# Performance work log

Hardware: AMD Instinct MI355X
Metric: run time of the kernel (lower is better)

The kernel has to match this reference:

```python
import jax, jax.numpy as jnp
import numpy as np

QP = 127.0          # signed symmetric 8-bit: Qp = 2**(8-1)-1
MIN_RANGE = 1e-6


def _ste_round(q):
    # round_pass: straight-through estimator round
    return q + jax.lax.stop_gradient(jnp.round(q) - q)


def _quant_per_token(x):
    # symmetric per-token: amax over last dim, keepdim
    s = jnp.clip(jnp.max(jnp.abs(x), axis=-1, keepdims=True), MIN_RANGE, None) / QP
    return _ste_round(x / s), s


def _quant_per_tensor(w):
    s = jnp.clip(jnp.max(jnp.abs(w)), MIN_RANGE, None) / QP
    return _ste_round(w / s), s


def _qlinear(x2d, w, b):
    # fake-quant linear: quantize act per-token, weight per-tensor,
    # int-domain matmul, bias added before dequant rescale (faithful to source)
    qx, sx = _quant_per_token(x2d)      # [N,K], [N,1]
    qw, sw = _quant_per_tensor(w)       # [M,K], scalar
    out = jnp.matmul(qx, qw.T) + b[None, :]
    return out * (sx * sw)              # [N,M]


def setup_inputs() -> dict:
    key = jax.random.key(0)
    k1, k2, k3, k4, k5 = jax.random.split(key, 5)
    B, S, D, H = 64, 197, 768, 3072
    return {
        "x": jax.random.normal(k1, (B, S, D), dtype=jnp.float32),
        "w1": jax.random.normal(k2, (H, D), dtype=jnp.float32) * 0.02,
        "b1": jax.random.normal(k3, (H,), dtype=jnp.float32) * 0.02,
        "w2": jax.random.normal(k4, (D, H), dtype=jnp.float32) * 0.02,
        "b2": jax.random.normal(k5, (D,), dtype=jnp.float32) * 0.02,
    }


def reference(x, w1, b1, w2, b2):
    B, S, D = x.shape
    x2d = x.reshape(-1, D)                         # view(-1, x.size(-1))
    h = _qlinear(x2d, w1, b1)                      # fc1
    h = jax.nn.gelu(h, approximate=False)          # ViT Mlp activation (exact GELU)
    o = _qlinear(h, w2, b2)                        # fc2
    return o.reshape(B, S, -1)
```

## Files before the change

### kernel.cpp

```cpp
#include <hip/hip_runtime.h>
#include <stdint.h>

#define QPF  127.0f
#define MINR 1e-6f

typedef int v4i __attribute__((ext_vector_type(4)));
typedef float f4v __attribute__((ext_vector_type(4)));
typedef _Float16 h4v __attribute__((ext_vector_type(4)));
typedef _Float16 h8 __attribute__((ext_vector_type(8)));
typedef signed char c8 __attribute__((ext_vector_type(8)));

__device__ __forceinline__ float wave_max64(float v) {
  v = fmaxf(v, __shfl_xor(v, 32, 64));
  v = fmaxf(v, __shfl_xor(v, 16, 64));
  v = fmaxf(v, __shfl_xor(v, 8, 64));
  v = fmaxf(v, __shfl_xor(v, 4, 64));
  v = fmaxf(v, __shfl_xor(v, 2, 64));
  v = fmaxf(v, __shfl_xor(v, 1, 64));
  return v;
}

__device__ __forceinline__ float gelu_exact(float x) {
  float z = fabsf(x) * 0.70710678118654752440f;
  float t = __builtin_amdgcn_rcpf(fmaf(0.3275911f, z, 1.0f));
  float p = fmaf(fmaf(fmaf(fmaf(1.061405429f, t, -1.453152027f), t,
                           1.421413741f), t, -0.284496736f), t, 0.254829592f) * t;
  float e = __expf(-z * z);
  float erfz = fmaf(-p, e, 1.0f);
  float cdf = fmaf(0.5f, copysignf(erfz, x), 0.5f);
  return x * cdf;
}

__device__ __forceinline__ void gl2lds16(const void* g, void* l) {
  __builtin_amdgcn_global_load_lds(
      (const __attribute__((address_space(1))) int*)g,
      (__attribute__((address_space(3))) int*)l,
      16, 0, 0);
}

__device__ __forceinline__ int xcd_swizzle(int flat, int nwg) {
  const int xcd = flat & 7;
  const int idx = flat >> 3;
  const int q = nwg >> 3, r = nwg & 7;
  const int base = (xcd < r) ? xcd * (q + 1) : r * (q + 1) + (xcd - r) * q;
  return base + idx;
}

__global__ __launch_bounds__(256) void pre_kernel(
    const float* __restrict__ w1, const float* __restrict__ w2, int n4,
    const float* __restrict__ x, signed char* __restrict__ qx,
    float* __restrict__ sx, unsigned* __restrict__ amaxh,
    float* __restrict__ partial, int K, int nTok) {
  __shared__ float red[4];
  const int b = blockIdx.x;
  const int tid = threadIdx.x;
  const int lane = tid & 63, wvi = tid >> 6;

  if (b < 1024) {
    const float4* w4 = (const float4*)(b < 512 ? w1 : w2);
    const int bb = b & 511;
    float m = 0.f;
    for (int i = bb * 256 + tid; i < n4; i += 512 * 256) {
      float4 v = w4[i];
      m = fmaxf(m, fmaxf(fmaxf(fabsf(v.x), fabsf(v.y)),
                         fmaxf(fabsf(v.z), fabsf(v.w))));
    }
    m = wave_max64(m);
    if (lane == 0) red[wvi] = m;
    __syncthreads();
    if (tid == 0)
      partial[b] = fmaxf(fmaxf(red[0], red[1]), fmaxf(red[2], red[3]));
  } else {
    const int token = (b - 1024) * 4 + wvi;
    if (token < nTok) {
      const int k4 = K >> 2;
      const float4* xr = (const float4*)(x + (size_t)token * K);
      float m = 0.f;
      for (int i = lane; i < k4; i += 64) {
        float4 v = xr[i];
        m = fmaxf(m, fmaxf(fmaxf(fabsf(v.x), fabsf(v.y)),
                           fmaxf(fabsf(v.z), fabsf(v.w))));
      }
      m = wave_max64(m);
      const float s = fmaxf(m, MINR) / QPF;
      const float rs = 1.0f / s;
      if (lane == 0) { sx[token] = s; amaxh[token] = 0u; }
      char4* q4 = (char4*)(qx + (size_t)token * K);
      for (int i = lane; i < k4; i += 64) {
        float4 v = xr[i];
        char4 c;
        c.x = (signed char)(int)rintf(v.x * rs);
        c.y = (signed char)(int)rintf(v.y * rs);
        c.z = (signed char)(int)rintf(v.z * rs);
        c.w = (signed char)(int)rintf(v.w * rs);
        q4[i] = c;
      }
    }
  }
}

__global__ __launch_bounds__(256) void wquant2_kernel(
    const float* __restrict__ w1, const float* __restrict__ w2, int n4,
    const float* __restrict__ partial, unsigned* __restrict__ wamax,
    signed char* __restrict__ q1, signed char* __restrict__ q2) {
  __shared__ float red[4];
  const int tid = threadIdx.x;
  const int lane = tid & 63, wvi = tid >> 6;
  const int y = blockIdx.y;
  float m = fmaxf(partial[y * 512 + tid], partial[y * 512 + 256 + tid]);
  m = wave_max64(m);
  if (lane == 0) red[wvi] = m;
  __syncthreads();
  const float M = fmaxf(fmaxf(red[0], red[1]), fmaxf(red[2], red[3]));
  if (blockIdx.x == 0 && tid == 0) wamax[y] = __float_as_uint(M);
  const float s = fmaxf(M, MINR) / QPF;
  const float rs = 1.0f / s;
  const float4* w4 = (const float4*)(y ? w2 : w1);
  char4* q4 = (char4*)(y ? q2 : q1);
  for (int i = blockIdx.x * 256 + tid; i < n4; i += gridDim.x * 256) {
    float4 v = w4[i];
    char4 c;
    c.x = (signed char)(int)rintf(v.x * rs);
    c.y = (signed char)(int)rintf(v.y * rs);
    c.z = (signed char)(int)rintf(v.z * rs);
    c.w = (signed char)(int)rintf(v.w * rs);
    q4[i] = c;
  }
}

__global__ __launch_bounds__(256) void hquant4_kernel(
    const _Float16* __restrict__ h, const unsigned* __restrict__ amaxbits,
    signed char* __restrict__ qh, float* __restrict__ sh, int K) {
  const int token = blockIdx.x * 4 + (threadIdx.x >> 6);
  const int lane = threadIdx.x & 63;
  const float s = fmaxf(__uint_as_float(amaxbits[token]), MINR) / QPF;
  const float rs = 1.0f / s;
  if (lane == 0) sh[token] = s;
  const h8* hr = (const h8*)(h + (size_t)token * K);
  c8* qr = (c8*)(qh + (size_t)token * K);
  for (int i = lane; i < (K >> 3); i += 64) {
    h8 v = hr[i];
    c8 c;
#pragma unroll
    for (int j = 0; j < 8; j++)
      c[j] = (signed char)(int)rintf((float)v[j] * rs);
    qr[i] = c;
  }
}

__global__ __launch_bounds__(256, 2) void gemm1_i8(
    const signed char* __restrict__ A, const signed char* __restrict__ B,
    const float* __restrict__ bias, const float* __restrict__ sA,
    const unsigned* __restrict__ sBbits, _Float16* __restrict__ out,
    unsigned* __restrict__ amax_out, int N, int K, int Mout) {
  __shared__ __align__(16) signed char lds[3 * 16384];

  const int t = threadIdx.x;
  const int lane = t & 63;
  const int wv = t >> 6;
  const int wm = wv >> 1;
  const int wn = wv & 1;

  const int nwg = gridDim.x * gridDim.y;
  const int wg = xcd_swizzle(blockIdx.x + gridDim.x * blockIdx.y, nwg);
  const int colBlk = (wg % gridDim.x) * 128;
  const int rowBlk = (wg / gridDim.x) * 128;

  int ar0 = rowBlk + wv * 16 + (lane >> 2);
  int ar1 = ar0 + 64;
  if (ar0 > N - 1) ar0 = N - 1;
  if (ar1 > N - 1) ar1 = N - 1;
  const int br0 = colBlk + wv * 16 + (lane >> 2);
  const int br1 = br0 + 64;
  const int kb = (((lane & 3) ^ ((lane >> 3) & 3)) * 16);

  const signed char* gA0 = A + (size_t)ar0 * K + kb;
  const signed char* gA1 = A + (size_t)ar1 * K + kb;
  const signed char* gB0 = B + (size_t)br0 * K + kb;
  const signed char* gB1 = B + (size_t)br1 * K + kb;

  const v4i vzero = {0, 0, 0, 0};
  v4i acc[4][4];
#pragma unroll
  for (int i = 0; i < 4; i++)
#pragma unroll
    for (int j = 0; j < 4; j++) acc[i][j] = vzero;

  const int swz = ((lane >> 4) ^ ((lane >> 1) & 3)) * 16;
  const int aoff = (wm * 64 + (lane & 15)) * 64 + swz;
  const int boff = (wn * 64 + (lane & 15)) * 64 + swz + 8192;

  const int T = K >> 6;

  auto issue = [&](int bufo) {
    signed char* a = lds + bufo + wv * 1024;
    gl2lds16(gA0, a);
    gl2lds16(gA1, a + 4096);
    gl2lds16(gB0, a + 8192);
    gl2lds16(gB1, a + 12288);
    gA0 += 64; gA1 += 64; gB0 += 64; gB1 += 64;
  };

  issue(0);
  issue(16384);

  int cur = 0;
  for (int kt = 0; kt < T; ++kt) {
    asm volatile("" ::: "memory");
    if (kt < T - 1)
      __builtin_amdgcn_s_waitcnt(0x0074);
    else
      __builtin_amdgcn_s_waitcnt(0x0070);
    __builtin_amdgcn_s_barrier();
    asm volatile("" ::: "memory");

    if (kt + 2 < T) {
      int pf = cur + 32768;
      if (pf >= 49152) pf -= 49152;
      issue(pf);
    }

    v4i a[4], b[4];
#pragma unroll
    for (int mi = 0; mi < 4; mi++)
      a[mi] = *(const v4i*)(lds + cur + aoff + mi * 1024);
#pragma unroll
    for (int ni = 0; ni < 4; ni++)
      b[ni] = *(const v4i*)(lds + cur + boff + ni * 1024);
#pragma unroll
    for (int mi = 0; mi < 4; mi++)
#pragma unroll
      for (int ni = 0; ni < 4; ni++)
        acc[mi][ni] = __builtin_amdgcn_mfma_i32_16x16x64_i8(b[ni], a[mi],
                                                            acc[mi][ni], 0, 0, 0);
    cur += 16384;
    if (cur >= 49152) cur = 0;
  }

  const float sB = fmaxf(__uint_as_float(*sBbits), MINR) / QPF;
  const int col0 = colBlk + wn * 64 + (lane >> 4) * 4;

  f4v bv[4];
#pragma unroll
  for (int ni = 0; ni < 4; ni++) bv[ni] = *(const f4v*)(bias + col0 + ni * 16);

#pragma unroll
  for (int mi = 0; mi < 4; mi++) {
    const int grow = rowBlk + wm * 64 + mi * 16 + (lane & 15);
    const float ss = ((grow < N) ? sA[grow] : 0.f) * sB;
    float rmax = 0.f;
#pragma unroll
    for (int ni = 0; ni < 4; ni++) {
      h4v hv;
#pragma unroll
      for (int r = 0; r < 4; r++) {
        float v = ((float)acc[mi][ni][r] + bv[ni][r]) * ss;
        v = gelu_exact(v);
        rmax = fmaxf(rmax, fabsf(v));
        hv[r] = (_Float16)v;
      }
      if (grow < N)
        *(h4v*)(out + (size_t)grow * Mout + col0 + ni * 16) = hv;
    }
    rmax = fmaxf(rmax, __shfl_xor(rmax, 16, 64));
    rmax = fmaxf(rmax, __shfl_xor(rmax, 32, 64));
    if (lane < 16 && grow < N)
      atomicMax(amax_out + grow, __float_as_uint(rmax));
  }
}

__global__ __launch_bounds__(256, 2) void gemm2_i8(
    const signed char* __restrict__ A, const signed char* __restrict__ B,
    const float* __restrict__ bias, const float* __restrict__ sA,
    const unsigned* __restrict__ sBbits, float* __restrict__ out,
    int N, int K, int Mout) {
  __shared__ __align__(16) signed char lds[3 * 16384];

  const int t = threadIdx.x;
  const int lane = t & 63;
  const int wv = t >> 6;
  const int wm = wv >> 1;
  const int wn = wv & 1;

  const int nwg = gridDim.x * gridDim.y;
  const int wg = xcd_swizzle(blockIdx.x + gridDim.x * blockIdx.y, nwg);
  const int colBlk = (wg % gridDim.x) * 128;
  const int rowBlk = (wg / gridDim.x) * 128;

  int ar0 = rowBlk + wv * 16 + (lane >> 2);
  int ar1 = ar0 + 64;
  if (ar0 > N - 1) ar0 = N - 1;
  if (ar1 > N - 1) ar1 = N - 1;
  const int br0 = colBlk + wv * 16 + (lane >> 2);
  const int br1 = br0 + 64;
  const int kb = (((lane & 3) ^ ((lane >> 3) & 3)) * 16);

  const signed char* gA0 = A + (size_t)ar0 * K + kb;
  const signed char* gA1 = A + (size_t)ar1 * K + kb;
  const signed char* gB0 = B + (size_t)br0 * K + kb;
  const signed char* gB1 = B + (size_t)br1 * K + kb;

  const v4i vzero = {0, 0, 0, 0};
  v4i acc[4][4];
#pragma unroll
  for (int i = 0; i < 4; i++)
#pragma unroll
    for (int j = 0; j < 4; j++) acc[i][j] = vzero;

  const int swz = ((lane >> 4) ^ ((lane >> 1) & 3)) * 16;
  const int aoff = (wm * 64 + (lane & 15)) * 64 + swz;
  const int boff = (wn * 64 + (lane & 15)) * 64 + swz + 8192;

  const int T = K >> 6;

  auto issue = [&](int bufo) {
    signed char* a = lds + bufo + wv * 1024;
    gl2lds16(gA0, a);
    gl2lds16(gA1, a + 4096);
    gl2lds16(gB0, a + 8192);
    gl2lds16(gB1, a + 12288);
    gA0 += 64; gA1 += 64; gB0 += 64; gB1 += 64;
  };

  issue(0);
  issue(16384);

  int cur = 0;
  for (int kt = 0; kt < T; ++kt) {
    asm volatile("" ::: "memory");
    if (kt < T - 1)
      __builtin_amdgcn_s_waitcnt(0x0074);
    else
      __builtin_amdgcn_s_waitcnt(0x0070);
    __builtin_amdgcn_s_barrier();
    asm volatile("" ::: "memory");

    if (kt + 2 < T) {
      int pf = cur + 32768;
      if (pf >= 49152) pf -= 49152;
      issue(pf);
    }

    v4i a[4], b[4];
#pragma unroll
    for (int mi = 0; mi < 4; mi++)
      a[mi] = *(const v4i*)(lds + cur + aoff + mi * 1024);
#pragma unroll
    for (int ni = 0; ni < 4; ni++)
      b[ni] = *(const v4i*)(lds + cur + boff + ni * 1024);
#pragma unroll
    for (int mi = 0; mi < 4; mi++)
#pragma unroll
      for (int ni = 0; ni < 4; ni++)
        acc[mi][ni] = __builtin_amdgcn_mfma_i32_16x16x64_i8(b[ni], a[mi],
                                                            acc[mi][ni], 0, 0, 0);
    cur += 16384;
    if (cur >= 49152) cur = 0;
  }

  const float sB = fmaxf(__uint_as_float(*sBbits), MINR) / QPF;
  const int col0 = colBlk + wn * 64 + (lane >> 4) * 4;

  f4v bv[4];
#pragma unroll
  for (int ni = 0; ni < 4; ni++) bv[ni] = *(const f4v*)(bias + col0 + ni * 16);

#pragma unroll
  for (int mi = 0; mi < 4; mi++) {
    const int grow = rowBlk + wm * 64 + mi * 16 + (lane & 15);
    const float ss = ((grow < N) ? sA[grow] : 0.f) * sB;
#pragma unroll
    for (int ni = 0; ni < 4; ni++) {
      f4v o;
#pragma unroll
      for (int r = 0; r < 4; r++)
        o[r] = ((float)acc[mi][ni][r] + bv[ni][r]) * ss;
      if (grow < N)
        *(f4v*)(out + (size_t)grow * Mout + col0 + ni * 16) = o;
    }
  }
}

extern "C" void kernel_launch(void* const* d_in, const int* in_sizes, int n_in,
                              void* d_out, int out_size, void* d_ws, size_t ws_size,
                              hipStream_t stream) {
  const float* x  = (const float*)d_in[0];
  const float* w1 = (const float*)d_in[1];
  const float* b1 = (const float*)d_in[2];
  const float* w2 = (const float*)d_in[3];
  const float* b2 = (const float*)d_in[4];

  const int H = in_sizes[2];
  const int D = in_sizes[4];
  const int N = in_sizes[0] / D;
  float* out = (float*)d_out;

  char* ws = (char*)d_ws;
  auto alloc = [&](size_t bytes) {
    char* p = ws;
    ws += (bytes + 255) & ~(size_t)255;
    return p;
  };
  signed char* qx  = (signed char*)alloc((size_t)N * D);
  signed char* qw1 = (signed char*)alloc((size_t)H * D);
  signed char* qw2 = (signed char*)alloc((size_t)H * D);
  signed char* qh  = (signed char*)alloc((size_t)N * H);
  float*    sx     = (float*)alloc((size_t)N * 4);
  float*    sh     = (float*)alloc((size_t)N * 4);
  unsigned* amaxh  = (unsigned*)alloc((size_t)N * 4);
  unsigned* wamax  = (unsigned*)alloc(256);
  float*    partial= (float*)alloc(1024 * 4);
  _Float16* h      = (_Float16*)alloc((size_t)N * H * 2);
  (void)ws_size;

  const int n4w = (H * D) >> 2;

  pre_kernel<<<1024 + (N + 3) / 4, 256, 0, stream>>>(w1, w2, n4w, x, qx, sx,
                                                     amaxh, partial, D, N);
  wquant2_kernel<<<dim3(512, 2), 256, 0, stream>>>(w1, w2, n4w, partial, wamax,
                                                   qw1, qw2);

  dim3 g1(H / 128, (N + 127) / 128);
  gemm1_i8<<<g1, 256, 0, stream>>>(qx, qw1, b1, sx, wamax + 0, h, amaxh,
                                   N, D, H);
  hquant4_kernel<<<N / 4, 256, 0, stream>>>(h, amaxh, qh, sh, H);

  dim3 g2(D / 128, (N + 127) / 128);
  gemm2_i8<<<g2, 256, 0, stream>>>(qh, qw2, b2, sh, wamax + 1, out, N, H, D);
}
```

Before: 234.3 us.

## Enlarge int8 GEMM tiles to 128x256 and 256x128 with six-load staging

```diff
diff --git a/kernel.cpp b/kernel.cpp
--- a/kernel.cpp
+++ b/kernel.cpp
@@ -153,7 +153,7 @@
     const float* __restrict__ bias, const float* __restrict__ sA,
     const unsigned* __restrict__ sBbits, _Float16* __restrict__ out,
     unsigned* __restrict__ amax_out, int N, int K, int Mout) {
-  __shared__ __align__(16) signed char lds[3 * 16384];
+  __shared__ __align__(16) signed char lds[3 * 24576];
 
   const int t = threadIdx.x;
   const int lane = t & 63;
@@ -163,86 +163,92 @@
 
   const int nwg = gridDim.x * gridDim.y;
   const int wg = xcd_swizzle(blockIdx.x + gridDim.x * blockIdx.y, nwg);
-  const int colBlk = (wg % gridDim.x) * 128;
+  const int colBlk = (wg % gridDim.x) * 256;
   const int rowBlk = (wg / gridDim.x) * 128;
 
-  int ar0 = rowBlk + wv * 16 + (lane >> 2);
-  int ar1 = ar0 + 64;
-  if (ar0 > N - 1) ar0 = N - 1;
-  if (ar1 > N - 1) ar1 = N - 1;
-  const int br0 = colBlk + wv * 16 + (lane >> 2);
-  const int br1 = br0 + 64;
   const int kb = (((lane & 3) ^ ((lane >> 3) & 3)) * 16);
-
-  const signed char* gA0 = A + (size_t)ar0 * K + kb;
-  const signed char* gA1 = A + (size_t)ar1 * K + kb;
-  const signed char* gB0 = B + (size_t)br0 * K + kb;
-  const signed char* gB1 = B + (size_t)br1 * K + kb;
+  const int rr = lane >> 2;
+
+  const signed char* gp[6];
+  int ldo[6];
+#pragma unroll
+  for (int j = 0; j < 6; j++) {
+    const int c = wv + 4 * j;
+    if (c < 8) {
+      int r = rowBlk + c * 16 + rr;
+      if (r > N - 1) r = N - 1;
+      gp[j] = A + (size_t)r * K + kb;
+      ldo[j] = c * 1024;
+    } else {
+      const int r = colBlk + (c - 8) * 16 + rr;
+      gp[j] = B + (size_t)r * K + kb;
+      ldo[j] = 8192 + (c - 8) * 1024;
+    }
+  }
 
   const v4i vzero = {0, 0, 0, 0};
-  v4i acc[4][4];
+  v4i acc[4][8];
 #pragma unroll
   for (int i = 0; i < 4; i++)
 #pragma unroll
-    for (int j = 0; j < 4; j++) acc[i][j] = vzero;
+    for (int j = 0; j < 8; j++) acc[i][j] = vzero;
 
   const int swz = ((lane >> 4) ^ ((lane >> 1) & 3)) * 16;
   const int aoff = (wm * 64 + (lane & 15)) * 64 + swz;
-  const int boff = (wn * 64 + (lane & 15)) * 64 + swz + 8192;
+  const int boff = 8192 + (wn * 128 + (lane & 15)) * 64 + swz;
 
   const int T = K >> 6;
 
   auto issue = [&](int bufo) {
-    signed char* a = lds + bufo + wv * 1024;
-    gl2lds16(gA0, a);
-    gl2lds16(gA1, a + 4096);
-    gl2lds16(gB0, a + 8192);
-    gl2lds16(gB1, a + 12288);
-    gA0 += 64; gA1 += 64; gB0 += 64; gB1 += 64;
+#pragma unroll
+    for (int j = 0; j < 6; j++) {
+      gl2lds16(gp[j], lds + bufo + ldo[j]);
+      gp[j] += 64;
+    }
   };
 
   issue(0);
-  issue(16384);
+  issue(24576);
 
   int cur = 0;
   for (int kt = 0; kt < T; ++kt) {
     asm volatile("" ::: "memory");
     if (kt < T - 1)
-      __builtin_amdgcn_s_waitcnt(0x0074);
+      __builtin_amdgcn_s_waitcnt(0x0076);
     else
       __builtin_amdgcn_s_waitcnt(0x0070);
     __builtin_amdgcn_s_barrier();
     asm volatile("" ::: "memory");
 
     if (kt + 2 < T) {
-      int pf = cur + 32768;
-      if (pf >= 49152) pf -= 49152;
+      int pf = cur + 49152;
+      if (pf >= 73728) pf -= 73728;
       issue(pf);
     }
 
-    v4i a[4], b[4];
+    v4i a[4], b[8];
 #pragma unroll
     for (int mi = 0; mi < 4; mi++)
       a[mi] = *(const v4i*)(lds + cur + aoff + mi * 1024);
 #pragma unroll
-    for (int ni = 0; ni < 4; ni++)
+    for (int ni = 0; ni < 8; ni++)
       b[ni] = *(const v4i*)(lds + cur + boff + ni * 1024);
 #pragma unroll
     for (int mi = 0; mi < 4; mi++)
 #pragma unroll
-      for (int ni = 0; ni < 4; ni++)
+      for (int ni = 0; ni < 8; ni++)
         acc[mi][ni] = __builtin_amdgcn_mfma_i32_16x16x64_i8(b[ni], a[mi],
                                                             acc[mi][ni], 0, 0, 0);
-    cur += 16384;
-    if (cur >= 49152) cur = 0;
+    cur += 24576;
+    if (cur >= 73728) cur = 0;
   }
 
   const float sB = fmaxf(__uint_as_float(*sBbits), MINR) / QPF;
-  const int col0 = colBlk + wn * 64 + (lane >> 4) * 4;
-
-  f4v bv[4];
-#pragma unroll
-  for (int ni = 0; ni < 4; ni++) bv[ni] = *(const f4v*)(bias + col0 + ni * 16);
+  const int col0 = colBlk + wn * 128 + (lane >> 4) * 4;
+
+  f4v bv[8];
+#pragma unroll
+  for (int ni = 0; ni < 8; ni++) bv[ni] = *(const f4v*)(bias + col0 + ni * 16);
 
 #pragma unroll
   for (int mi = 0; mi < 4; mi++) {
@@ -250,7 +256,7 @@
     const float ss = ((grow < N) ? sA[grow] : 0.f) * sB;
     float rmax = 0.f;
 #pragma unroll
-    for (int ni = 0; ni < 4; ni++) {
+    for (int ni = 0; ni < 8; ni++) {
       h4v hv;
 #pragma unroll
       for (int r = 0; r < 4; r++) {
@@ -274,7 +280,7 @@
     const float* __restrict__ bias, const float* __restrict__ sA,
     const unsigned* __restrict__ sBbits, float* __restrict__ out,
     int N, int K, int Mout) {
-  __shared__ __align__(16) signed char lds[3 * 16384];
+  __shared__ __align__(16) signed char lds[3 * 24576];
 
   const int t = threadIdx.x;
   const int lane = t & 63;
@@ -285,77 +291,83 @@
   const int nwg = gridDim.x * gridDim.y;
   const int wg = xcd_swizzle(blockIdx.x + gridDim.x * blockIdx.y, nwg);
   const int colBlk = (wg % gridDim.x) * 128;
-  const int rowBlk = (wg / gridDim.x) * 128;
-
-  int ar0 = rowBlk + wv * 16 + (lane >> 2);
-  int ar1 = ar0 + 64;
-  if (ar0 > N - 1) ar0 = N - 1;
-  if (ar1 > N - 1) ar1 = N - 1;
-  const int br0 = colBlk + wv * 16 + (lane >> 2);
-  const int br1 = br0 + 64;
+  const int rowBlk = (wg / gridDim.x) * 256;
+
   const int kb = (((lane & 3) ^ ((lane >> 3) & 3)) * 16);
-
-  const signed char* gA0 = A + (size_t)ar0 * K + kb;
-  const signed char* gA1 = A + (size_t)ar1 * K + kb;
-  const signed char* gB0 = B + (size_t)br0 * K + kb;
-  const signed char* gB1 = B + (size_t)br1 * K + kb;
+  const int rr = lane >> 2;
+
+  const signed char* gp[6];
+  int ldo[6];
+#pragma unroll
+  for (int j = 0; j < 6; j++) {
+    const int c = wv + 4 * j;
+    if (c < 16) {
+      int r = rowBlk + c * 16 + rr;
+      if (r > N - 1) r = N - 1;
+      gp[j] = A + (size_t)r * K + kb;
+      ldo[j] = c * 1024;
+    } else {
+      const int r = colBlk + (c - 16) * 16 + rr;
+      gp[j] = B + (size_t)r * K + kb;
+      ldo[j] = 16384 + (c - 16) * 1024;
+    }
+  }
 
   const v4i vzero = {0, 0, 0, 0};
-  v4i acc[4][4];
-#pragma unroll
-  for (int i = 0; i < 4; i++)
+  v4i acc[8][4];
+#pragma unroll
+  for (int i = 0; i < 8; i++)
 #pragma unroll
     for (int j = 0; j < 4; j++) acc[i][j] = vzero;
 
   const int swz = ((lane >> 4) ^ ((lane >> 1) & 3)) * 16;
-  const int aoff = (wm * 64 + (lane & 15)) * 64 + swz;
-  const int boff = (wn * 64 + (lane & 15)) * 64 + swz + 8192;
+  const int aoff = (wm * 128 + (lane & 15)) * 64 + swz;
+  const int boff = 16384 + (wn * 64 + (lane & 15)) * 64 + swz;
 
   const int T = K >> 6;
 
   auto issue = [&](int bufo) {
-    signed char* a = lds + bufo + wv * 1024;
-    gl2lds16(gA0, a);
-    gl2lds16(gA1, a + 4096);
-    gl2lds16(gB0, a + 8192);
-    gl2lds16(gB1, a + 12288);
-    gA0 += 64; gA1 += 64; gB0 += 64; gB1 += 64;
+#pragma unroll
+    for (int j = 0; j < 6; j++) {
+      gl2lds16(gp[j], lds + bufo + ldo[j]);
+      gp[j] += 64;
+    }
   };
 
   issue(0);
-  issue(16384);
+  issue(24576);
 
   int cur = 0;
   for (int kt = 0; kt < T; ++kt) {
     asm volatile("" ::: "memory");
     if (kt < T - 1)
-      __builtin_amdgcn_s_waitcnt(0x0074);
+      __builtin_amdgcn_s_waitcnt(0x0076);
     else
       __builtin_amdgcn_s_waitcnt(0x0070);
     __builtin_amdgcn_s_barrier();
     asm volatile("" ::: "memory");
 
     if (kt + 2 < T) {
-      int pf = cur + 32768;
-      if (pf >= 49152) pf -= 49152;
+      int pf = cur + 49152;
+      if (pf >= 73728) pf -= 73728;
       issue(pf);
     }
 
-    v4i a[4], b[4];
-#pragma unroll
-    for (int mi = 0; mi < 4; mi++)
+    v4i a[8], b[4];
+#pragma unroll
+    for (int mi = 0; mi < 8; mi++)
       a[mi] = *(const v4i*)(lds + cur + aoff + mi * 1024);
 #pragma unroll
     for (int ni = 0; ni < 4; ni++)
       b[ni] = *(const v4i*)(lds + cur + boff + ni * 1024);
 #pragma unroll
-    for (int mi = 0; mi < 4; mi++)
+    for (int mi = 0; mi < 8; mi++)
 #pragma unroll
       for (int ni = 0; ni < 4; ni++)
         acc[mi][ni] = __builtin_amdgcn_mfma_i32_16x16x64_i8(b[ni], a[mi],
                                                             acc[mi][ni], 0, 0, 0);
-    cur += 16384;
-    if (cur >= 49152) cur = 0;
+    cur += 24576;
+    if (cur >= 73728) cur = 0;
   }
 
   const float sB = fmaxf(__uint_as_float(*sBbits), MINR) / QPF;
@@ -366,8 +378,8 @@
   for (int ni = 0; ni < 4; ni++) bv[ni] = *(const f4v*)(bias + col0 + ni * 16);
 
 #pragma unroll
-  for (int mi = 0; mi < 4; mi++) {
-    const int grow = rowBlk + wm * 64 + mi * 16 + (lane & 15);
+  for (int mi = 0; mi < 8; mi++) {
+    const int grow = rowBlk + wm * 128 + mi * 16 + (lane & 15);
     const float ss = ((grow < N) ? sA[grow] : 0.f) * sB;
 #pragma unroll
     for (int ni = 0; ni < 4; ni++) {
@@ -420,11 +432,11 @@
   wquant2_kernel<<<dim3(512, 2), 256, 0, stream>>>(w1, w2, n4w, partial, wamax,
                                                    qw1, qw2);
 
-  dim3 g1(H / 128, (N + 127) / 128);
+  dim3 g1(H / 256, (N + 127) / 128);
   gemm1_i8<<<g1, 256, 0, stream>>>(qx, qw1, b1, sx, wamax + 0, h, amaxh,
                                    N, D, H);
   hquant4_kernel<<<N / 4, 256, 0, stream>>>(h, amaxh, qh, sh, H);
 
-  dim3 g2(D / 128, (N + 127) / 128);
+  dim3 g2(D / 128, (N + 255) / 256);
   gemm2_i8<<<g2, 256, 0, stream>>>(qh, qw2, b2, sh, wamax + 1, out, N, H, D);
 }
```

New measurement: 238.6 us. About the same (+1.8%).

## Replace LDS-staged triple buffering with direct global-to-register double-buffered loads

Applied to the files above, without the earlier changes.

```diff
diff --git a/kernel.cpp b/kernel.cpp
--- a/kernel.cpp
+++ b/kernel.cpp
@@ -29,13 +29,6 @@
   float erfz = fmaf(-p, e, 1.0f);
   float cdf = fmaf(0.5f, copysignf(erfz, x), 0.5f);
   return x * cdf;
-}
-
-__device__ __forceinline__ void gl2lds16(const void* g, void* l) {
-  __builtin_amdgcn_global_load_lds(
-      (const __attribute__((address_space(1))) int*)g,
-      (__attribute__((address_space(3))) int*)l,
-      16, 0, 0);
 }
 
 __device__ __forceinline__ int xcd_swizzle(int flat, int nwg) {
@@ -148,13 +141,23 @@
   }
 }
 
+#define GLOADF(XA, WB, KB)                                        \
+  _Pragma("unroll") for (int i_ = 0; i_ < 4; i_++)                \
+      XA[i_] = *(const v4i*)(A + aofs[i_] + (KB));                \
+  _Pragma("unroll") for (int i_ = 0; i_ < 4; i_++)                \
+      WB[i_] = *(const v4i*)(B + bofs[i_] + (KB));
+
+#define GMMA(XA, WB)                                              \
+  _Pragma("unroll") for (int mi_ = 0; mi_ < 4; mi_++)             \
+  _Pragma("unroll") for (int ni_ = 0; ni_ < 4; ni_++)             \
+      acc[mi_][ni_] = __builtin_amdgcn_mfma_i32_16x16x64_i8(      \
+          WB[ni_], XA[mi_], acc[mi_][ni_], 0, 0, 0);
+
 __global__ __launch_bounds__(256, 2) void gemm1_i8(
     const signed char* __restrict__ A, const signed char* __restrict__ B,
     const float* __restrict__ bias, const float* __restrict__ sA,
     const unsigned* __restrict__ sBbits, _Float16* __restrict__ out,
     unsigned* __restrict__ amax_out, int N, int K, int Mout) {
-  __shared__ __align__(16) signed char lds[3 * 16384];
-
   const int t = threadIdx.x;
   const int lane = t & 63;
   const int wv = t >> 6;
@@ -166,18 +169,20 @@
   const int colBlk = (wg % gridDim.x) * 128;
   const int rowBlk = (wg / gridDim.x) * 128;
 
-  int ar0 = rowBlk + wv * 16 + (lane >> 2);
-  int ar1 = ar0 + 64;
-  if (ar0 > N - 1) ar0 = N - 1;
-  if (ar1 > N - 1) ar1 = N - 1;
-  const int br0 = colBlk + wv * 16 + (lane >> 2);
-  const int br1 = br0 + 64;
-  const int kb = (((lane & 3) ^ ((lane >> 3) & 3)) * 16);
-
-  const signed char* gA0 = A + (size_t)ar0 * K + kb;
-  const signed char* gA1 = A + (size_t)ar1 * K + kb;
-  const signed char* gB0 = B + (size_t)br0 * K + kb;
-  const signed char* gB1 = B + (size_t)br1 * K + kb;
+  const int koff = (lane >> 4) * 16;
+
+  int aofs[4], bofs[4];
+#pragma unroll
+  for (int mi = 0; mi < 4; mi++) {
+    int r = rowBlk + wm * 64 + mi * 16 + (lane & 15);
+    if (r > N - 1) r = N - 1;
+    aofs[mi] = r * K + koff;
+  }
+#pragma unroll
+  for (int ni = 0; ni < 4; ni++) {
+    const int r = colBlk + wn * 64 + ni * 16 + (lane & 15);
+    bofs[ni] = r * K + koff;
+  }
 
   const v4i vzero = {0, 0, 0, 0};
   v4i acc[4][4];
@@ -186,55 +191,15 @@
 #pragma unroll
     for (int j = 0; j < 4; j++) acc[i][j] = vzero;
 
-  const int swz = ((lane >> 4) ^ ((lane >> 1) & 3)) * 16;
-  const int aoff = (wm * 64 + (lane & 15)) * 64 + swz;
-  const int boff = (wn * 64 + (lane & 15)) * 64 + swz + 8192;
-
   const int T = K >> 6;
 
-  auto issue = [&](int bufo) {
-    signed char* a = lds + bufo + wv * 1024;
-    gl2lds16(gA0, a);
-    gl2lds16(gA1, a + 4096);
-    gl2lds16(gB0, a + 8192);
-    gl2lds16(gB1, a + 12288);
-    gA0 += 64; gA1 += 64; gB0 += 64; gB1 += 64;
-  };
-
-  issue(0);
-  issue(16384);
-
-  int cur = 0;
-  for (int kt = 0; kt < T; ++kt) {
-    asm volatile("" ::: "memory");
-    if (kt < T - 1)
-      __builtin_amdgcn_s_waitcnt(0x0074);
-    else
-      __builtin_amdgcn_s_waitcnt(0x0070);
-    __builtin_amdgcn_s_barrier();
-    asm volatile("" ::: "memory");
-
-    if (kt + 2 < T) {
-      int pf = cur + 32768;
-      if (pf >= 49152) pf -= 49152;
-      issue(pf);
-    }
-
-    v4i a[4], b[4];
-#pragma unroll
-    for (int mi = 0; mi < 4; mi++)
-      a[mi] = *(const v4i*)(lds + cur + aoff + mi * 1024);
-#pragma unroll
-    for (int ni = 0; ni < 4; ni++)
-      b[ni] = *(const v4i*)(lds + cur + boff + ni * 1024);
-#pragma unroll
-    for (int mi = 0; mi < 4; mi++)
-#pragma unroll
-      for (int ni = 0; ni < 4; ni++)
-        acc[mi][ni] = __builtin_amdgcn_mfma_i32_16x16x64_i8(b[ni], a[mi],
-                                                            acc[mi][ni], 0, 0, 0);
-    cur += 16384;
-    if (cur >= 49152) cur = 0;
+  v4i xa0[4], wb0[4], xa1[4], wb1[4];
+  GLOADF(xa0, wb0, 0)
+  for (int kt = 0; kt < T; kt += 2) {
+    GLOADF(xa1, wb1, (kt + 1) * 64)
+    GMMA(xa0, wb0)
+    if (kt + 2 < T) { GLOADF(xa0, wb0, (kt + 2) * 64) }
+    GMMA(xa1, wb1)
   }
 
   const float sB = fmaxf(__uint_as_float(*sBbits), MINR) / QPF;
@@ -274,8 +239,6 @@
     const float* __restrict__ bias, const float* __restrict__ sA,
     const unsigned* __restrict__ sBbits, float* __restrict__ out,
     int N, int K, int Mout) {
-  __shared__ __align__(16) signed char lds[3 * 16384];
-
   const int t = threadIdx.x;
   const int lane = t & 63;
   const int wv = t >> 6;
@@ -287,18 +250,20 @@
   const int colBlk = (wg % gridDim.x) * 128;
   const int rowBlk = (wg / gridDim.x) * 128;
 
-  int ar0 = rowBlk + wv * 16 + (lane >> 2);
-  int ar1 = ar0 + 64;
-  if (ar0 > N - 1) ar0 = N - 1;
-  if (ar1 > N - 1) ar1 = N - 1;
-  const int br0 = colBlk + wv * 16 + (lane >> 2);
-  const int br1 = br0 + 64;
-  const int kb = (((lane & 3) ^ ((lane >> 3) & 3)) * 16);
-
-  const signed char* gA0 = A + (size_t)ar0 * K + kb;
-  const signed char* gA1 = A + (size_t)ar1 * K + kb;
-  const signed char* gB0 = B + (size_t)br0 * K + kb;
-  const signed char* gB1 = B + (size_t)br1 * K + kb;
+  const int koff = (lane >> 4) * 16;
+
+  int aofs[4], bofs[4];
+#pragma unroll
+  for (int mi = 0; mi < 4; mi++) {
+    int r = rowBlk + wm * 64 + mi * 16 + (lane & 15);
+    if (r > N - 1) r = N - 1;
+    aofs[mi] = r * K + koff;
+  }
+#pragma unroll
+  for (int ni = 0; ni < 4; ni++) {
+    const int r = colBlk + wn * 64 + ni * 16 + (lane & 15);
+    bofs[ni] = r * K + koff;
+  }
 
   const v4i vzero = {0, 0, 0, 0};
   v4i acc[4][4];
@@ -307,55 +272,15 @@
 #pragma unroll
     for (int j = 0; j < 4; j++) acc[i][j] = vzero;
 
-  const int swz = ((lane >> 4) ^ ((lane >> 1) & 3)) * 16;
-  const int aoff = (wm * 64 + (lane & 15)) * 64 + swz;
-  const int boff = (wn * 64 + (lane & 15)) * 64 + swz + 8192;
-
   const int T = K >> 6;
 
-  auto issue = [&](int bufo) {
-    signed char* a = lds + bufo + wv * 1024;
-    gl2lds16(gA0, a);
-    gl2lds16(gA1, a + 4096);
-    gl2lds16(gB0, a + 8192);
-    gl2lds16(gB1, a + 12288);
-    gA0 += 64; gA1 += 64; gB0 += 64; gB1 += 64;
-  };
-
-  issue(0);
-  issue(16384);
-
-  int cur = 0;
-  for (int kt = 0; kt < T; ++kt) {
-    asm volatile("" ::: "memory");
-    if (kt < T - 1)
-      __builtin_amdgcn_s_waitcnt(0x0074);
-    else
-      __builtin_amdgcn_s_waitcnt(0x0070);
-    __builtin_amdgcn_s_barrier();
-    asm volatile("" ::: "memory");
-
-    if (kt + 2 < T) {
-      int pf = cur + 32768;
-      if (pf >= 49152) pf -= 49152;
-      issue(pf);
-    }
-
-    v4i a[4], b[4];
-#pragma unroll
-    for (int mi = 0; mi < 4; mi++)
-      a[mi] = *(const v4i*)(lds + cur + aoff + mi * 1024);
-#pragma unroll
-    for (int ni = 0; ni < 4; ni++)
-      b[ni] = *(const v4i*)(lds + cur + boff + ni * 1024);
-#pragma unroll
-    for (int mi = 0; mi < 4; mi++)
-#pragma unroll
-      for (int ni = 0; ni < 4; ni++)
-        acc[mi][ni] = __builtin_amdgcn_mfma_i32_16x16x64_i8(b[ni], a[mi],
-                                                            acc[mi][ni], 0, 0, 0);
-    cur += 16384;
-    if (cur >= 49152) cur = 0;
+  v4i xa0[4], wb0[4], xa1[4], wb1[4];
+  GLOADF(xa0, wb0, 0)
+  for (int kt = 0; kt < T; kt += 2) {
+    GLOADF(xa1, wb1, (kt + 1) * 64)
+    GMMA(xa0, wb0)
+    if (kt + 2 < T) { GLOADF(xa0, wb0, (kt + 2) * 64) }
+    GMMA(xa1, wb1)
   }
 
   const float sB = fmaxf(__uint_as_float(*sBbits), MINR) / QPF;
```

Measured after the change: 383.6 us. 1.64x slower.

## Fuse hidden-activation quantization into gemm1 via last-block-per-panel counter

Applied to the files above, without the earlier changes.

```diff
diff --git a/kernel.cpp b/kernel.cpp
--- a/kernel.cpp
+++ b/kernel.cpp
@@ -50,13 +50,15 @@
     const float* __restrict__ w1, const float* __restrict__ w2, int n4,
     const float* __restrict__ x, signed char* __restrict__ qx,
     float* __restrict__ sx, unsigned* __restrict__ amaxh,
-    float* __restrict__ partial, int K, int nTok) {
+    float* __restrict__ partial, unsigned* __restrict__ panel_cnt,
+    int K, int nTok) {
   __shared__ float red[4];
   const int b = blockIdx.x;
   const int tid = threadIdx.x;
   const int lane = tid & 63, wvi = tid >> 6;
 
   if (b < 1024) {
+    if (b == 0 && tid < 128) panel_cnt[tid] = 0u;
     const float4* w4 = (const float4*)(b < 512 ? w1 : w2);
     const int bb = b & 511;
     float m = 0.f;
@@ -128,32 +130,15 @@
   }
 }
 
-__global__ __launch_bounds__(256) void hquant4_kernel(
-    const _Float16* __restrict__ h, const unsigned* __restrict__ amaxbits,
-    signed char* __restrict__ qh, float* __restrict__ sh, int K) {
-  const int token = blockIdx.x * 4 + (threadIdx.x >> 6);
-  const int lane = threadIdx.x & 63;
-  const float s = fmaxf(__uint_as_float(amaxbits[token]), MINR) / QPF;
-  const float rs = 1.0f / s;
-  if (lane == 0) sh[token] = s;
-  const h8* hr = (const h8*)(h + (size_t)token * K);
-  c8* qr = (c8*)(qh + (size_t)token * K);
-  for (int i = lane; i < (K >> 3); i += 64) {
-    h8 v = hr[i];
-    c8 c;
-#pragma unroll
-    for (int j = 0; j < 8; j++)
-      c[j] = (signed char)(int)rintf((float)v[j] * rs);
-    qr[i] = c;
-  }
-}
-
 __global__ __launch_bounds__(256, 2) void gemm1_i8(
     const signed char* __restrict__ A, const signed char* __restrict__ B,
     const float* __restrict__ bias, const float* __restrict__ sA,
-    const unsigned* __restrict__ sBbits, _Float16* __restrict__ out,
-    unsigned* __restrict__ amax_out, int N, int K, int Mout) {
+    const unsigned* __restrict__ sBbits, _Float16* __restrict__ h,
+    signed char* __restrict__ qh, float* __restrict__ sh,
+    unsigned* __restrict__ amax_out, unsigned* __restrict__ panel_cnt,
+    int N, int K, int Mout) {
   __shared__ __align__(16) signed char lds[3 * 16384];
+  __shared__ unsigned tick;
 
   const int t = threadIdx.x;
   const int lane = t & 63;
@@ -164,7 +149,8 @@
   const int nwg = gridDim.x * gridDim.y;
   const int wg = xcd_swizzle(blockIdx.x + gridDim.x * blockIdx.y, nwg);
   const int colBlk = (wg % gridDim.x) * 128;
-  const int rowBlk = (wg / gridDim.x) * 128;
+  const int panelIdx = wg / gridDim.x;
+  const int rowBlk = panelIdx * 128;
 
   int ar0 = rowBlk + wv * 16 + (lane >> 2);
   int ar1 = ar0 + 64;
@@ -260,12 +246,44 @@
         hv[r] = (_Float16)v;
       }
       if (grow < N)
-        *(h4v*)(out + (size_t)grow * Mout + col0 + ni * 16) = hv;
+        *(h4v*)(h + (size_t)grow * Mout + col0 + ni * 16) = hv;
     }
     rmax = fmaxf(rmax, __shfl_xor(rmax, 16, 64));
     rmax = fmaxf(rmax, __shfl_xor(rmax, 32, 64));
     if (lane < 16 && grow < N)
       atomicMax(amax_out + grow, __float_as_uint(rmax));
+  }
+
+  __syncthreads();
+  if (t == 0) {
+    __threadfence();
+    tick = __hip_atomic_fetch_add(panel_cnt + panelIdx, 1u,
+                                  __ATOMIC_ACQ_REL, __HIP_MEMORY_SCOPE_AGENT);
+  }
+  __syncthreads();
+
+  if (tick == (unsigned)(gridDim.x - 1)) {
+    __threadfence();
+    const int sub = t & 7;
+    for (int tk = t >> 3; tk < 128; tk += 32) {
+      const int tok = rowBlk + tk;
+      if (tok < N) {
+        const float am = __uint_as_float(atomicOr(amax_out + tok, 0u));
+        const float s = fmaxf(am, MINR) / QPF;
+        const float rs = 1.0f / s;
+        if (sub == 0) sh[tok] = s;
+        const h8* hr = (const h8*)(h + (size_t)tok * Mout);
+        c8* qr = (c8*)(qh + (size_t)tok * Mout);
+        for (int i = sub; i < (Mout >> 3); i += 8) {
+          h8 v = hr[i];
+          c8 c;
+#pragma unroll
+          for (int j = 0; j < 8; j++)
+            c[j] = (signed char)(int)rintf((float)v[j] * rs);
+          qr[i] = c;
+        }
+      }
+    }
   }
 }
 
@@ -410,20 +428,20 @@
   unsigned* amaxh  = (unsigned*)alloc((size_t)N * 4);
   unsigned* wamax  = (unsigned*)alloc(256);
   float*    partial= (float*)alloc(1024 * 4);
+  unsigned* pcnt   = (unsigned*)alloc(512);
   _Float16* h      = (_Float16*)alloc((size_t)N * H * 2);
   (void)ws_size;
 
   const int n4w = (H * D) >> 2;
 
   pre_kernel<<<1024 + (N + 3) / 4, 256, 0, stream>>>(w1, w2, n4w, x, qx, sx,
-                                                     amaxh, partial, D, N);
+                                                     amaxh, partial, pcnt, D, N);
   wquant2_kernel<<<dim3(512, 2), 256, 0, stream>>>(w1, w2, n4w, partial, wamax,
                                                    qw1, qw2);
 
   dim3 g1(H / 128, (N + 127) / 128);
-  gemm1_i8<<<g1, 256, 0, stream>>>(qx, qw1, b1, sx, wamax + 0, h, amaxh,
-                                   N, D, H);
-  hquant4_kernel<<<N / 4, 256, 0, stream>>>(h, amaxh, qh, sh, H);
+  gemm1_i8<<<g1, 256, 0, stream>>>(qx, qw1, b1, sx, wamax + 0, h, qh, sh,
+                                   amaxh, pcnt, N, D, H);
 
   dim3 g2(D / 128, (N + 127) / 128);
   gemm2_i8<<<g2, 256, 0, stream>>>(qh, qw2, b2, sh, wamax + 1, out, N, H, D);
```

Result: slower. 511.2 us (+118.2%).
